# Kernel optimization log

Measured on AMD Instinct MI355X. Metric: run time of the kernel, lower is better.

Reference implementation:

```python
import jax, jax.numpy as jnp
import numpy as np

N_AGENTS, BATCH, SDIM, ADIM = 8, 16384, 64, 16
HID, HEADS = 128, 4
ATT_D = HID // HEADS  # 32
EPS = 1e-5


def _bn(x):
    # BatchNorm1d(affine=False), training-mode stats over batch axis (axis=1), biased var
    m = x.mean(axis=1, keepdims=True)
    v = ((x - m) ** 2).mean(axis=1, keepdims=True)
    return (x - m) * jax.lax.rsqrt(v + EPS)


def setup_inputs() -> dict:
    key = jax.random.key(0)
    ks = jax.random.split(key, 16)
    sc = lambda *sh: 1.0 / np.sqrt(sh[-2] if len(sh) > 1 else sh[-1])
    inp = {
        "s": jax.random.normal(ks[0], (N_AGENTS, BATCH, SDIM), jnp.float32),
        "a": jax.random.uniform(ks[1], (N_AGENTS, BATCH, ADIM), jnp.float32),
        # per-agent sa encoder (Attention_Actor): Linear(sdim+adim, hid)
        "W_sa": jax.random.normal(ks[2], (N_AGENTS, SDIM + ADIM, HID), jnp.float32) * (1.0 / np.sqrt(SDIM + ADIM)),
        "b_sa": jnp.zeros((N_AGENTS, HID), jnp.float32),
        # per-agent state encoder: Linear(sdim, hid)
        "W_se": jax.random.normal(ks[3], (N_AGENTS, SDIM, HID), jnp.float32) * (1.0 / np.sqrt(SDIM)),
        "b_se": jnp.zeros((N_AGENTS, HID), jnp.float32),
        # per-head key/selector (no bias) and value (with bias) extractors, shared across agents
        "Wk": jax.random.normal(ks[4], (HEADS, HID, ATT_D), jnp.float32) * (1.0 / np.sqrt(HID)),
        "Wsel": jax.random.normal(ks[5], (HEADS, HID, ATT_D), jnp.float32) * (1.0 / np.sqrt(HID)),
        "Wv": jax.random.normal(ks[6], (HEADS, HID, ATT_D), jnp.float32) * (1.0 / np.sqrt(HID)),
        "bv": jnp.zeros((HEADS, ATT_D), jnp.float32),
        # per-agent critic: Linear(2*hid, hid) -> LeakyReLU -> Linear(hid, adim)
        "Wc1": jax.random.normal(ks[7], (N_AGENTS, 2 * HID, HID), jnp.float32) * (1.0 / np.sqrt(2 * HID)),
        "bc1": jnp.zeros((N_AGENTS, HID), jnp.float32),
        "Wc2": jax.random.normal(ks[8], (N_AGENTS, HID, ADIM), jnp.float32) * (1.0 / np.sqrt(HID)),
        "bc2": jnp.zeros((N_AGENTS, ADIM), jnp.float32),
    }
    return inp


def reference(s, a, W_sa, b_sa, W_se, b_se, Wk, Wsel, Wv, bv, Wc1, bc1, Wc2, bc2):
    lrelu = jax.nn.leaky_relu  # slope 0.01 like nn.LeakyReLU default
    # sa encodings: BN -> Linear -> LeakyReLU, per agent  [N,B,H]
    sa = _bn(jnp.concatenate([s, a], axis=-1))
    e = lrelu(jnp.einsum('nbi,nih->nbh', sa, W_sa) + b_sa[:, None, :])
    # state encodings  [N,B,H]
    se = lrelu(jnp.einsum('nbi,nih->nbh', _bn(s), W_se) + b_se[:, None, :])
    # per-head projections  [P,N,B,D]
    keys = jnp.einsum('nbh,phd->pnbd', e, Wk)
    vals = lrelu(jnp.einsum('nbh,phd->pnbd', e, Wv) + bv[:, None, None, :])
    sel = jnp.einsum('nbh,phd->pnbd', se, Wsel)
    # attention of agent i over agents j != i  [P,N,N,B]
    logits = jnp.einsum('pibd,pjbd->pijb', sel, keys) / np.sqrt(ATT_D).astype(np.float32)
    self_mask = jnp.eye(N_AGENTS, dtype=bool)[None, :, :, None]
    w = jax.nn.softmax(jnp.where(self_mask, -1e9, logits), axis=2)
    other = jnp.einsum('pijb,pjbd->pibd', w, vals)  # [P,N,B,D]
    other_flat = jnp.transpose(other, (1, 2, 0, 3)).reshape(N_AGENTS, BATCH, HEADS * ATT_D)
    # critic: concat(s_enc, head values) -> MLP -> gather Q at argmax action
    critic_in = jnp.concatenate([se, other_flat], axis=-1)  # [N,B,2H]
    h = lrelu(jnp.einsum('nbi,nih->nbh', critic_in, Wc1) + bc1[:, None, :])
    all_q = jnp.einsum('nbh,nho->nbo', h, Wc2) + bc2[:, None, :]  # [N,B,adim]
    int_acs = jnp.argmax(a, axis=-1)[..., None]  # [N,B,1]
    q = jnp.take_along_axis(all_q, int_acs, axis=-1)  # [N,B,1]
    return q
```

## Files before the change

kernel.cpp:

```cpp
#include <hip/hip_runtime.h>


typedef unsigned short u16;
typedef unsigned int u32;

#define NA 8
#define BATCH 16384
#define SD 64
#define AD 16
#define IND 80
#define HID 128
#define HEADS 4
#define ATT 32
#define EPS 1e-5f
#define KP 136
#define KP3 104
#define KPS 72
#define SP 34
#define VTS2 136
#define WBS 24

using short8 = __attribute__((ext_vector_type(8))) short;
using float4f = __attribute__((ext_vector_type(4))) float;
using uint4v = __attribute__((ext_vector_type(4))) u32;
#define MFMA16(a, b, c) __builtin_amdgcn_mfma_f32_16x16x32_bf16((a), (b), (c), 0, 0, 0)

__device__ __forceinline__ float bf2f(u16 u) { union { u32 i; float f; } v; v.i = ((u32)u) << 16; return v.f; }
__device__ __forceinline__ float lo2f(u32 w) { union { u32 i; float f; } v; v.i = w << 16; return v.f; }
__device__ __forceinline__ float hi2f(u32 w) { union { u32 i; float f; } v; v.i = w & 0xffff0000u; return v.f; }
__device__ __forceinline__ u16 f2bf(float f) {
  union { float f; u32 i; } v; v.f = f;
  u32 x = v.i;
  x += 0x7fffu + ((x >> 16) & 1u);
  return (u16)(x >> 16);
}
__device__ __forceinline__ float lrelu(float x) { return x > 0.f ? x : 0.01f * x; }
__device__ __forceinline__ float ldin(const void* p, size_t i, bool bf) {
  return bf ? bf2f(((const u16*)p)[i]) : ((const float*)p)[i];
}
__device__ __forceinline__ u16 ldbf(const void* p, size_t i, bool bf) {
  return bf ? ((const u16*)p)[i] : f2bf(((const float*)p)[i]);
}
__device__ __forceinline__ short8 lds_s8(const u16* p) {
  union { short8 v; u32 u[4]; } t;
  const u32* q = (const u32*)p;
  t.u[0] = q[0]; t.u[1] = q[1]; t.u[2] = q[2]; t.u[3] = q[3];
  return t.v;
}
__device__ __forceinline__ void barlg() {
  asm volatile("s_waitcnt lgkmcnt(0)" ::: "memory");
  __builtin_amdgcn_s_barrier();
}

__global__ __launch_bounds__(256) void k_prep2(
    const void* __restrict__ s, const void* __restrict__ a,
    const void* __restrict__ Wsa, const void* __restrict__ Wse,
    const void* __restrict__ Wsl, const void* __restrict__ Wk, const void* __restrict__ Wv,
    const void* __restrict__ Wc1,
    int* __restrict__ flag, float* __restrict__ part,
    u16* __restrict__ Wsa_t, u16* __restrict__ Wse_t, u16* __restrict__ Wp_t, u16* __restrict__ Wc1t) {
  __shared__ u16 T[80 * 130];
  __shared__ float S0[256], Q0[256], S1[256], Q1[256];
  __shared__ int cnt[2];
  int tid = threadIdx.x;
  if (tid < 2) cnt[tid] = 0;
  __syncthreads();
  {
    u32 wv = ((const u32*)s)[tid];
    u32 lo = wv & 0xffffu, e = (lo >> 7) & 0xffu;
    if (lo == 0u || lo == 0x8000u) atomicAdd(&cnt[1], 1);
    else if (e < 0x70u || e > 0x8fu) atomicAdd(&cnt[0], 1);
  }
  __syncthreads();
  bool bf = !(cnt[0] >= 64 || cnt[1] >= 192);
  if (blockIdx.x == 0 && tid == 0) *flag = bf ? 1 : 0;
  int blkr = blockIdx.x;
  if (blkr < 2048) {
    int n = blkr >> 8, c = blkr & 255, b0 = c << 6;
    float* p = part + (size_t)(n * 256 + c) * 160;
    {
      int f2 = tid & 31, rg = tid >> 5;
      float s0 = 0.f, s1 = 0.f, q0 = 0.f, q1 = 0.f;
      #pragma unroll
      for (int i = 0; i < 8; i++) {
        int b = b0 + rg + 8 * i;
        float x0, x1;
        if (bf) { u32 wv = ((const u32*)s)[((size_t)n * BATCH + b) * 32 + f2]; x0 = lo2f(wv); x1 = hi2f(wv); }
        else { const float* sf = (const float*)s + ((size_t)n * BATCH + b) * 64 + 2 * f2; x0 = sf[0]; x1 = sf[1]; }
        s0 += x0; q0 += x0 * x0; s1 += x1; q1 += x1 * x1;
      }
      S0[tid] = s0; Q0[tid] = q0; S1[tid] = s1; Q1[tid] = q1;
    }
    __syncthreads();
    if (tid < 64) {
      int f2 = tid >> 1, odd = tid & 1;
      float S = 0.f, Q = 0.f;
      #pragma unroll
      for (int rg = 0; rg < 8; rg++) {
        int ix = rg * 32 + f2;
        S += odd ? S1[ix] : S0[ix];
        Q += odd ? Q1[ix] : Q0[ix];
      }
      p[tid * 2] = S; p[tid * 2 + 1] = Q;
    }
    __syncthreads();
    {
      int f2 = tid & 7, rg = tid >> 3;
      float s0 = 0.f, s1 = 0.f, q0 = 0.f, q1 = 0.f;
      #pragma unroll
      for (int i = 0; i < 2; i++) {
        int b = b0 + rg + 32 * i;
        float x0, x1;
        if (bf) { u32 wv = ((const u32*)a)[((size_t)n * BATCH + b) * 8 + f2]; x0 = lo2f(wv); x1 = hi2f(wv); }
        else { const float* af = (const float*)a + ((size_t)n * BATCH + b) * 16 + 2 * f2; x0 = af[0]; x1 = af[1]; }
        s0 += x0; q0 += x0 * x0; s1 += x1; q1 += x1 * x1;
      }
      S0[tid] = s0; Q0[tid] = q0; S1[tid] = s1; Q1[tid] = q1;
    }
    __syncthreads();
    if (tid < 16) {
      int f2 = tid >> 1, odd = tid & 1;
      float S = 0.f, Q = 0.f;
      #pragma unroll
      for (int rg = 0; rg < 32; rg++) {
        int ix = rg * 8 + f2;
        S += odd ? S1[ix] : S0[ix];
        Q += odd ? Q1[ix] : Q0[ix];
      }
      p[(SD + tid) * 2] = S; p[(SD + tid) * 2 + 1] = Q;
    }
    return;
  }
  int blk = blkr - 2048;
  if (blk < 32) {
    int n = blk >> 2, k0 = (blk & 3) * 64;
    for (int i = tid; i < 64 * 128; i += 256) {
      int kr = i >> 7, cc = i & 127;
      T[kr * 130 + cc] = ldbf(Wc1, ((size_t)n * 256 + k0 + kr) * 128 + cc, bf);
    }
    __syncthreads();
    for (int i = tid; i < 128 * 64; i += 256) {
      int col = i >> 6, kk = i & 63;
      Wc1t[((size_t)n * 128 + col) * 256 + k0 + kk] = T[kk * 130 + col];
    }
  } else if (blk < 40) {
    int n = blk - 32;
    for (int i = tid; i < 80 * 128; i += 256) {
      int kr = i >> 7, cc = i & 127;
      T[kr * 130 + cc] = ldbf(Wsa, ((size_t)n * IND + kr) * 128 + cc, bf);
    }
    __syncthreads();
    for (int i = tid; i < 128 * KP3; i += 256) {
      int col = i / KP3, k = i - col * KP3;
      Wsa_t[((size_t)n * 128 + col) * KP3 + k] = (k < IND) ? T[k * 130 + col] : (u16)0;
    }
  } else if (blk < 48) {
    int n = blk - 40;
    for (int i = tid; i < 64 * 128; i += 256) {
      int kr = i >> 7, cc = i & 127;
      T[kr * 130 + cc] = ldbf(Wse, ((size_t)n * SD + kr) * 128 + cc, bf);
    }
    __syncthreads();
    for (int i = tid; i < 128 * KPS; i += 256) {
      int col = i / KPS, k = i - col * KPS;
      Wse_t[((size_t)n * 128 + col) * KPS + k] = (k < SD) ? T[k * 130 + col] : (u16)0;
    }
  } else {
    int pm = blk - 48, p = pm / 3, mat = pm - 3 * p;
    const void* W = (mat == 0) ? Wsl : (mat == 1) ? Wk : Wv;
    for (int i = tid; i < 128 * 32; i += 256) {
      int kr = i >> 5, d = i & 31;
      T[kr * 34 + d] = ldbf(W, ((size_t)p * HID + kr) * ATT + d, bf);
    }
    __syncthreads();
    for (int i = tid; i < 32 * KP; i += 256) {
      int d = i / KP, k = i - d * KP;
      Wp_t[((size_t)mat * HID + p * ATT + d) * KP + k] = (k < HID) ? T[k * 34 + d] : (u16)0;
    }
  }
}

__global__ __launch_bounds__(256) void k_fin(const float* __restrict__ part, float* __restrict__ mst_g) {
  int n = blockIdx.x;
  int t = threadIdx.x;
  if (t < 160) {
    const float* p = part + (size_t)n * 256 * 160 + t;
    float acc = 0.f;
    #pragma unroll 8
    for (int c = 0; c < 256; c++) acc += p[(size_t)c * 160];
    float other = __shfl_xor(acc, 1);
    if ((t & 1) == 0) {
      float mean = acc * (1.f / BATCH);
      float var = other * (1.f / BATCH) - mean * mean;
      mst_g[(size_t)n * 160 + t] = mean;
      mst_g[(size_t)n * 160 + t + 1] = rsqrtf(var + EPS);
    }
  }
}

__global__ __launch_bounds__(512, 4) void k_fused(
    const void* __restrict__ s, const void* __restrict__ a,
    const u16* __restrict__ Wsa_t, const void* __restrict__ bsa,
    const u16* __restrict__ Wse_t, const void* __restrict__ bse,
    const u16* __restrict__ Wp_t, const void* __restrict__ bv_g,
    const float* __restrict__ mst_g, const int* __restrict__ flag,
    u16* __restrict__ SEo, u16* __restrict__ OT2) {
  __shared__ __align__(16) u16 A[128 * KP];
  __shared__ __align__(16) u16 scr[128 * SP];
  __shared__ __align__(16) u16 valt[ATT * VTS2];
  __shared__ u16 wb[128 * WBS];
  __shared__ float mst[NA * 160];
  bool bf = (*flag != 0);
  int tid = threadIdx.x;
  int B0 = blockIdx.x * 16;
  int w = tid >> 6, lane = tid & 63, q = lane >> 4, rl = lane & 15;
  for (int i = tid; i < NA * 160; i += 512) mst[i] = mst_g[i];
  barlg();
  for (int i = tid; i < 128 * 32; i += 512) {
    int row = i >> 5, kp = i & 31;
    int ag = row >> 4, bi = row & 15;
    float x0, x1;
    if (bf) { u32 wv = ((const u32*)s)[((size_t)ag * BATCH + B0 + bi) * 32 + kp]; x0 = lo2f(wv); x1 = hi2f(wv); }
    else { const float* sf = (const float*)s + ((size_t)ag * BATCH + B0 + bi) * 64 + 2 * kp; x0 = sf[0]; x1 = sf[1]; }
    int k = 2 * kp;
    const float* m = &mst[ag * 160];
    u32 o = (u32)f2bf((x0 - m[k * 2]) * m[k * 2 + 1]) |
            ((u32)f2bf((x1 - m[k * 2 + 2]) * m[k * 2 + 3]) << 16);
    *(u32*)&A[row * KP + k] = o;
  }
  for (int i = tid; i < 128 * 8; i += 512) {
    int row = i >> 3, kp = i & 7;
    int ag = row >> 4, bi = row & 15;
    float x0, x1;
    if (bf) { u32 wv = ((const u32*)a)[((size_t)ag * BATCH + B0 + bi) * 8 + kp]; x0 = lo2f(wv); x1 = hi2f(wv); }
    else { const float* af = (const float*)a + ((size_t)ag * BATCH + B0 + bi) * 16 + 2 * kp; x0 = af[0]; x1 = af[1]; }
    int k = SD + 2 * kp;
    const float* m = &mst[ag * 160];
    u32 o = (u32)f2bf((x0 - m[k * 2]) * m[k * 2 + 1]) |
            ((u32)f2bf((x1 - m[k * 2 + 2]) * m[k * 2 + 3]) << 16);
    *(u32*)&A[row * KP + k] = o;
  }
  for (int i = tid; i < 128 * 8; i += 512) {
    int row = i >> 3, c2 = i & 7;
    *(u32*)&A[row * KP + IND + 2 * c2] = 0u;
  }
  barlg();
  const int n = w;
  const u16* WS = Wse_t + (size_t)n * HID * KPS;
  const u16* WA = Wsa_t + (size_t)n * HID * KP3;
  float4f accS[8] = {};
  #pragma unroll
  for (int kc = 0; kc < 2; kc++) {
    short8 a0 = *(const short8*)&A[(w * 16 + rl) * KP + kc * 32 + q * 8];
    #pragma unroll
    for (int nt = 0; nt < 8; nt++) {
      short8 bb = *(const short8*)(WS + (size_t)(nt * 16 + rl) * KPS + kc * 32 + q * 8);
      accS[nt] = MFMA16(a0, bb, accS[nt]);
    }
  }
  float4f accE[8] = {};
  #pragma unroll
  for (int kc = 0; kc < 3; kc++) {
    short8 a0 = *(const short8*)&A[(w * 16 + rl) * KP + kc * 32 + q * 8];
    #pragma unroll
    for (int nt = 0; nt < 8; nt++) {
      short8 bb = *(const short8*)(WA + (size_t)(nt * 16 + rl) * KP3 + kc * 32 + q * 8);
      accE[nt] = MFMA16(a0, bb, accE[nt]);
    }
  }
  barlg();
  #pragma unroll
  for (int nt = 0; nt < 8; nt++) {
    int col = nt * 16 + rl;
    float bias = ldin(bse, n * HID + col, bf);
    #pragma unroll
    for (int r = 0; r < 4; r++) {
      int bi = q * 4 + r;
      u16 v = f2bf(lrelu(accS[nt][r] + bias));
      A[(w * 16 + bi) * KP + col] = v;
      SEo[((size_t)n * BATCH + B0 + bi) * HID + col] = v;
    }
  }
  const u16* WSL = Wp_t;
  const u16* WKm = Wp_t + (size_t)HID * KP;
  const u16* WVm = Wp_t + (size_t)2 * HID * KP;
  short8 saf[HEADS];
  #pragma unroll
  for (int p = 0; p < HEADS; p++) {
    float4f ac[2] = {};
    #pragma unroll
    for (int kc = 0; kc < 4; kc++) {
      short8 af = *(const short8*)&A[(w * 16 + rl) * KP + kc * 32 + q * 8];
      #pragma unroll
      for (int nt = 0; nt < 2; nt++) {
        short8 bl = *(const short8*)(WSL + (size_t)(p * ATT + nt * 16 + rl) * KP + kc * 32 + q * 8);
        ac[nt] = MFMA16(af, bl, ac[nt]);
      }
    }
    #pragma unroll
    for (int nt = 0; nt < 2; nt++)
      #pragma unroll
      for (int r = 0; r < 4; r++) {
        int bi = q * 4 + r, d = nt * 16 + rl;
        scr[(bi * 8 + w) * SP + d] = f2bf(ac[nt][r]);
      }
    barlg();
    saf[p] = lds_s8(&scr[(w * 16 + rl) * SP + q * 8]);
    barlg();
  }
  #pragma unroll
  for (int nt = 0; nt < 8; nt++) {
    int col = nt * 16 + rl;
    float bias = ldin(bsa, n * HID + col, bf);
    #pragma unroll
    for (int r = 0; r < 4; r++)
      A[(w * 16 + q * 4 + r) * KP + col] = f2bf(lrelu(accE[nt][r] + bias));
  }
  const float scale = 0.17677669529663687f;
  #pragma unroll
  for (int p = 0; p < HEADS; p++) {
    float4f ak[2] = {}, av[2] = {};
    #pragma unroll
    for (int kc = 0; kc < 4; kc++) {
      short8 af = *(const short8*)&A[(w * 16 + rl) * KP + kc * 32 + q * 8];
      #pragma unroll
      for (int nt = 0; nt < 2; nt++) {
        short8 bk = *(const short8*)(WKm + (size_t)(p * ATT + nt * 16 + rl) * KP + kc * 32 + q * 8);
        ak[nt] = MFMA16(af, bk, ak[nt]);
        short8 bv8 = *(const short8*)(WVm + (size_t)(p * ATT + nt * 16 + rl) * KP + kc * 32 + q * 8);
        av[nt] = MFMA16(af, bv8, av[nt]);
      }
    }
    #pragma unroll
    for (int nt = 0; nt < 2; nt++) {
      int d = nt * 16 + rl;
      float bvv = ldin(bv_g, p * ATT + d, bf);
      #pragma unroll
      for (int r = 0; r < 4; r++) {
        int bi = q * 4 + r, iRow = bi * 8 + w;
        scr[iRow * SP + d] = f2bf(ak[nt][r]);
        valt[d * VTS2 + iRow] = f2bf(lrelu(av[nt][r] + bvv));
      }
    }
    barlg();
    short8 sa = saf[p];
    short8 kb = lds_s8(&scr[(w * 16 + rl) * SP + q * 8]);
    float4f zc = {};
    float4f c = MFMA16(sa, kb, zc);
    int nn = rl;
    #pragma unroll
    for (int r = 0; r < 4; r++) {
      int row = q * 4 + r;
      float x = c[r] * scale;
      if (row == nn) x = -1e9f;
      float mx = x;
      mx = fmaxf(mx, __shfl_xor(mx, 1));
      mx = fmaxf(mx, __shfl_xor(mx, 2));
      mx = fmaxf(mx, __shfl_xor(mx, 4));
      float e = __expf(x - mx);
      float ssum = e;
      ssum += __shfl_xor(ssum, 1);
      ssum += __shfl_xor(ssum, 2);
      ssum += __shfl_xor(ssum, 4);
      float wv = e / ssum;
      if ((row >> 3) != (nn >> 3)) wv = 0.f;
      wb[(w * 16 + row) * WBS + nn] = f2bf(wv);
    }
    short8 aw;
    if (q < 2) aw = *(const short8*)&wb[(w * 16 + rl) * WBS + q * 8];
    else { short8 z = {}; aw = z; }
    float4f o[2] = {};
    #pragma unroll
    for (int nt = 0; nt < 2; nt++) {
      short8 bv8 = lds_s8(&valt[(nt * 16 + rl) * VTS2 + w * 16 + (q & 1) * 8]);
      o[nt] = MFMA16(aw, bv8, o[nt]);
    }
    #pragma unroll
    for (int nt = 0; nt < 2; nt++)
      #pragma unroll
      for (int r = 0; r < 4; r++) {
        int row = q * 4 + r;
        int rp = w * 16 + (row >> 3) * 8 + (row & 7);
        OT2[((size_t)blockIdx.x * 128 + rp) * HID + p * ATT + nt * 16 + rl] = f2bf(o[nt][r]);
      }
    barlg();
  }
}

__global__ __launch_bounds__(256) void k_critic2(
    const u16* __restrict__ SEi, const u16* __restrict__ OT, const void* __restrict__ a_g,
    const u16* __restrict__ Wc1t, const void* __restrict__ bc1_g,
    const void* __restrict__ Wc2_g, const void* __restrict__ bc2_g,
    const int* __restrict__ flag, void* __restrict__ qo) {
  __shared__ __align__(16) u16 Xt[128 * KP];
  __shared__ float wc2f[HID * AD];
  __shared__ float bc1f[HID];
  __shared__ int amax[128];
  bool bf = (*flag != 0);
  int tid = threadIdx.x;
  int n = blockIdx.y;
  int b0 = blockIdx.x * 128;
  int w = tid >> 6, lane = tid & 63, q = lane >> 4, rl = lane & 15;
  if (tid < HID) bc1f[tid] = ldin(bc1_g, n * HID + tid, bf);
  {
    int b = tid >> 1, half = tid & 1;
    float best; int bi;
    if (bf) {
      const uint4v* pa = (const uint4v*)((const u32*)a_g + ((size_t)n * BATCH + b0 + b) * 8 + half * 4);
      uint4v x = *pa;
      float v[8] = {lo2f(x[0]), hi2f(x[0]), lo2f(x[1]), hi2f(x[1]),
                    lo2f(x[2]), hi2f(x[2]), lo2f(x[3]), hi2f(x[3])};
      best = v[0]; bi = 0;
      #pragma unroll
      for (int j = 1; j < 8; j++) if (v[j] > best) { best = v[j]; bi = j; }
    } else {
      const float* pa = (const float*)a_g + ((size_t)n * BATCH + b0 + b) * 16 + half * 8;
      float4f v0 = *(const float4f*)pa, v1 = *(const float4f*)(pa + 4);
      float v[8] = {v0[0], v0[1], v0[2], v0[3], v1[0], v1[1], v1[2], v1[3]};
      best = v[0]; bi = 0;
      #pragma unroll
      for (int j = 1; j < 8; j++) if (v[j] > best) { best = v[j]; bi = j; }
    }
    float ob = __shfl_xor(best, 1);
    int obi = __shfl_xor(bi, 1);
    if (half == 0) amax[b] = (ob > best) ? (obi + 8) : bi;
  }
  for (int idx = tid; idx < HID * AD; idx += 256)
    wc2f[idx] = ldin(Wc2_g, (size_t)n * HID * AD + idx, bf);
  const u16* WT = Wc1t + (size_t)n * HID * 256;

  float4f acc[8][2] = {};
  for (int ph = 0; ph < 2; ph++) {
    for (int idx = tid; idx < 128 * 64; idx += 256) {
      int row = idx >> 6, c = idx & 63;
      u32 wv;
      if (ph == 0) wv = ((const u32*)SEi)[((size_t)n * BATCH + b0 + row) * 64 + c];
      else         wv = ((const u32*)OT)[((size_t)(b0 + row) * NA + n) * 64 + c];
      ((u32*)&Xt[row * KP])[c] = wv;
    }
    barlg();
    #pragma unroll
    for (int kc = 0; kc < 4; kc++) {
      int ko = ph * HID + kc * 32;
      short8 bb0 = *(const short8*)(WT + (size_t)(w * 32 + rl) * 256 + ko + q * 8);
      short8 bb1 = *(const short8*)(WT + (size_t)(w * 32 + 16 + rl) * 256 + ko + q * 8);
      #pragma unroll
      for (int mt = 0; mt < 8; mt++) {
        short8 af = *(const short8*)&Xt[(mt * 16 + rl) * KP + kc * 32 + q * 8];
        acc[mt][0] = MFMA16(af, bb0, acc[mt][0]);
        acc[mt][1] = MFMA16(af, bb1, acc[mt][1]);
      }
    }
    barlg();
  }
  u16* ht = Xt;
  #pragma unroll
  for (int mt = 0; mt < 8; mt++)
    #pragma unroll
    for (int nt = 0; nt < 2; nt++)
      #pragma unroll
      for (int r = 0; r < 4; r++) {
        int row = mt * 16 + q * 4 + r, col = w * 32 + nt * 16 + rl;
        ht[row * KP + col] = f2bf(lrelu(acc[mt][nt][r] + bc1f[col]));
      }
  barlg();
  {
    int b = tid >> 1, half = tid & 1;
    int col = amax[b];
    float acq = 0.f;
    const u16* hr = &ht[b * KP + half * 64];
    const float* wz = &wc2f[(half * 64) * AD + col];
    #pragma unroll
    for (int kk = 0; kk < 8; kk++) {
      short8 hv = lds_s8(hr + kk * 8);
      #pragma unroll
      for (int j = 0; j < 8; j++)
        acq = fmaf(bf2f((u16)hv[j]), wz[(kk * 8 + j) * AD], acq);
    }
    acq += __shfl_xor(acq, 1);
    if (half == 0) {
      float v = acq + ldin(bc2_g, n * AD + col, bf);
      size_t oidx = (size_t)n * BATCH + b0 + b;
      if (bf) ((u16*)qo)[oidx] = f2bf(v);
      else    ((float*)qo)[oidx] = v;
    }
  }
}

extern "C" void kernel_launch(void* const* d_in, const int* in_sizes, int n_in,
                              void* d_out, int out_size, void* d_ws, size_t ws_size,
                              hipStream_t stream) {
  const void* s   = d_in[0];
  const void* a   = d_in[1];
  const void* Wsa = d_in[2];
  const void* bsa = d_in[3];
  const void* Wse = d_in[4];
  const void* bse = d_in[5];
  const void* Wk  = d_in[6];
  const void* Wsl = d_in[7];
  const void* Wv  = d_in[8];
  const void* bv  = d_in[9];
  const void* Wc1 = d_in[10];
  const void* bc1 = d_in[11];
  const void* Wc2 = d_in[12];
  const void* bc2 = d_in[13];

  char* ws = (char*)d_ws;
  int*   flag  = (int*)ws;
  float* part  = (float*)(ws + 1024);
  float* mst_g = (float*)(ws + 1311744);
  u16*   Wsa_t = (u16*)(ws + 1316864);
  u16*   Wse_t = (u16*)(ws + 1529856);
  u16*   Wp_t  = (u16*)(ws + 1677312);
  u16*   Wc1t  = (u16*)(ws + 1781760);
  u16*   SEb   = (u16*)(ws + 2306048);
  u16*   OT2   = (u16*)(ws + 2306048 + 1ull * 33554432ull);

  k_prep2<<<2108, 256, 0, stream>>>(s, a, Wsa, Wse, Wsl, Wk, Wv, Wc1,
                                    flag, part, Wsa_t, Wse_t, Wp_t, Wc1t);
  k_fin<<<NA, 256, 0, stream>>>(part, mst_g);
  k_fused<<<BATCH / 16, 512, 0, stream>>>(s, a, Wsa_t, bsa, Wse_t, bse, Wp_t, bv,
                                          mst_g, flag, SEb, OT2);
  k_critic2<<<dim3(BATCH / 128, NA), 256, 0, stream>>>(SEb, OT2, a, Wc1t, bc1, Wc2, bc2, flag, d_out);
}
```

Baseline: 256.3 us.

## Batch all head projections in fused kernel to cut per-head barriers

Restructures the fused attention kernel so the selector, key and value projections for all four heads are computed up front in register accumulators. The results are staged once into two full-size LDS buffers, replacing the small per-head scratch and value-transpose buffers. This removes the two or three block barriers per head and lets each A-fragment load feed all head MFMAs. In exchange, register pressure rises sharply (24 float4 accumulators plus the earlier ones), which could cause spills or lower occupancy under the 512-thread, 4-block launch bound. LDS footprint also grows.

```diff
diff --git a/kernel.cpp b/kernel.cpp
--- a/kernel.cpp
+++ b/kernel.cpp
@@ -16,8 +16,6 @@
 #define KP 136
 #define KP3 104
 #define KPS 72
-#define SP 34
-#define VTS2 136
 #define WBS 24
 
 using short8 = __attribute__((ext_vector_type(8))) short;
@@ -198,7 +196,7 @@
   }
 }
 
-__global__ __launch_bounds__(512, 4) void k_fused(
+__global__ __launch_bounds__(512, 4) void k_fused2(
     const void* __restrict__ s, const void* __restrict__ a,
     const u16* __restrict__ Wsa_t, const void* __restrict__ bsa,
     const u16* __restrict__ Wse_t, const void* __restrict__ bse,
@@ -206,8 +204,7 @@
     const float* __restrict__ mst_g, const int* __restrict__ flag,
     u16* __restrict__ SEo, u16* __restrict__ OT2) {
   __shared__ __align__(16) u16 A[128 * KP];
-  __shared__ __align__(16) u16 scr[128 * SP];
-  __shared__ __align__(16) u16 valt[ATT * VTS2];
+  __shared__ __align__(16) u16 Bt[128 * KP];
   __shared__ u16 wb[128 * WBS];
   __shared__ float mst[NA * 160];
   bool bf = (*flag != 0);
@@ -272,79 +269,81 @@
   #pragma unroll
   for (int nt = 0; nt < 8; nt++) {
     int col = nt * 16 + rl;
-    float bias = ldin(bse, n * HID + col, bf);
+    float biasS = ldin(bse, n * HID + col, bf);
+    float biasE = ldin(bsa, n * HID + col, bf);
     #pragma unroll
     for (int r = 0; r < 4; r++) {
       int bi = q * 4 + r;
-      u16 v = f2bf(lrelu(accS[nt][r] + bias));
-      A[(w * 16 + bi) * KP + col] = v;
+      u16 v = f2bf(lrelu(accS[nt][r] + biasS));
+      Bt[(w * 16 + bi) * KP + col] = v;
       SEo[((size_t)n * BATCH + B0 + bi) * HID + col] = v;
+      A[(w * 16 + bi) * KP + col] = f2bf(lrelu(accE[nt][r] + biasE));
     }
   }
   const u16* WSL = Wp_t;
   const u16* WKm = Wp_t + (size_t)HID * KP;
   const u16* WVm = Wp_t + (size_t)2 * HID * KP;
-  short8 saf[HEADS];
-  #pragma unroll
-  for (int p = 0; p < HEADS; p++) {
-    float4f ac[2] = {};
-    #pragma unroll
-    for (int kc = 0; kc < 4; kc++) {
-      short8 af = *(const short8*)&A[(w * 16 + rl) * KP + kc * 32 + q * 8];
+  float4f aSL[4][2] = {};
+  #pragma unroll
+  for (int kc = 0; kc < 4; kc++) {
+    short8 af = *(const short8*)&Bt[(w * 16 + rl) * KP + kc * 32 + q * 8];
+    #pragma unroll
+    for (int p = 0; p < HEADS; p++)
       #pragma unroll
       for (int nt = 0; nt < 2; nt++) {
         short8 bl = *(const short8*)(WSL + (size_t)(p * ATT + nt * 16 + rl) * KP + kc * 32 + q * 8);
-        ac[nt] = MFMA16(af, bl, ac[nt]);
-      }
-    }
-    #pragma unroll
-    for (int nt = 0; nt < 2; nt++)
-      #pragma unroll
-      for (int r = 0; r < 4; r++) {
-        int bi = q * 4 + r, d = nt * 16 + rl;
-        scr[(bi * 8 + w) * SP + d] = f2bf(ac[nt][r]);
-      }
-    barlg();
-    saf[p] = lds_s8(&scr[(w * 16 + rl) * SP + q * 8]);
-    barlg();
-  }
-  #pragma unroll
-  for (int nt = 0; nt < 8; nt++) {
-    int col = nt * 16 + rl;
-    float bias = ldin(bsa, n * HID + col, bf);
-    #pragma unroll
-    for (int r = 0; r < 4; r++)
-      A[(w * 16 + q * 4 + r) * KP + col] = f2bf(lrelu(accE[nt][r] + bias));
-  }
-  const float scale = 0.17677669529663687f;
-  #pragma unroll
-  for (int p = 0; p < HEADS; p++) {
-    float4f ak[2] = {}, av[2] = {};
-    #pragma unroll
-    for (int kc = 0; kc < 4; kc++) {
-      short8 af = *(const short8*)&A[(w * 16 + rl) * KP + kc * 32 + q * 8];
+        aSL[p][nt] = MFMA16(af, bl, aSL[p][nt]);
+      }
+  }
+  float4f aK[4][2] = {}, aV[4][2] = {};
+  #pragma unroll
+  for (int kc = 0; kc < 4; kc++) {
+    short8 af = *(const short8*)&A[(w * 16 + rl) * KP + kc * 32 + q * 8];
+    #pragma unroll
+    for (int p = 0; p < HEADS; p++)
       #pragma unroll
       for (int nt = 0; nt < 2; nt++) {
         short8 bk = *(const short8*)(WKm + (size_t)(p * ATT + nt * 16 + rl) * KP + kc * 32 + q * 8);
-        ak[nt] = MFMA16(af, bk, ak[nt]);
+        aK[p][nt] = MFMA16(af, bk, aK[p][nt]);
         short8 bv8 = *(const short8*)(WVm + (size_t)(p * ATT + nt * 16 + rl) * KP + kc * 32 + q * 8);
-        av[nt] = MFMA16(af, bv8, av[nt]);
-      }
-    }
+        aV[p][nt] = MFMA16(af, bv8, aV[p][nt]);
+      }
+  }
+  barlg();
+  #pragma unroll
+  for (int p = 0; p < HEADS; p++)
+    #pragma unroll
+    for (int nt = 0; nt < 2; nt++)
+      #pragma unroll
+      for (int r = 0; r < 4; r++) {
+        int iRow = (q * 4 + r) * 8 + w, col = p * ATT + nt * 16 + rl;
+        Bt[iRow * KP + col] = f2bf(aSL[p][nt][r]);
+        A[iRow * KP + col] = f2bf(aK[p][nt][r]);
+      }
+  barlg();
+  short8 saf[HEADS];
+  #pragma unroll
+  for (int p = 0; p < HEADS; p++)
+    saf[p] = lds_s8(&Bt[(w * 16 + rl) * KP + p * ATT + q * 8]);
+  barlg();
+  #pragma unroll
+  for (int p = 0; p < HEADS; p++)
     #pragma unroll
     for (int nt = 0; nt < 2; nt++) {
       int d = nt * 16 + rl;
       float bvv = ldin(bv_g, p * ATT + d, bf);
       #pragma unroll
       for (int r = 0; r < 4; r++) {
-        int bi = q * 4 + r, iRow = bi * 8 + w;
-        scr[iRow * SP + d] = f2bf(ak[nt][r]);
-        valt[d * VTS2 + iRow] = f2bf(lrelu(av[nt][r] + bvv));
-      }
-    }
-    barlg();
+        int iRow = (q * 4 + r) * 8 + w;
+        Bt[(p * ATT + d) * KP + iRow] = f2bf(lrelu(aV[p][nt][r] + bvv));
+      }
+    }
+  barlg();
+  const float scale = 0.17677669529663687f;
+  #pragma unroll
+  for (int p = 0; p < HEADS; p++) {
     short8 sa = saf[p];
-    short8 kb = lds_s8(&scr[(w * 16 + rl) * SP + q * 8]);
+    short8 kb = lds_s8(&A[(w * 16 + rl) * KP + p * ATT + q * 8]);
     float4f zc = {};
     float4f c = MFMA16(sa, kb, zc);
     int nn = rl;
@@ -372,7 +371,7 @@
     float4f o[2] = {};
     #pragma unroll
     for (int nt = 0; nt < 2; nt++) {
-      short8 bv8 = lds_s8(&valt[(nt * 16 + rl) * VTS2 + w * 16 + (q & 1) * 8]);
+      short8 bv8 = lds_s8(&Bt[(p * ATT + nt * 16 + rl) * KP + w * 16 + (q & 1) * 8]);
       o[nt] = MFMA16(aw, bv8, o[nt]);
     }
     #pragma unroll
@@ -383,7 +382,6 @@
         int rp = w * 16 + (row >> 3) * 8 + (row & 7);
         OT2[((size_t)blockIdx.x * 128 + rp) * HID + p * ATT + nt * 16 + rl] = f2bf(o[nt][r]);
       }
-    barlg();
   }
 }
 
@@ -519,7 +517,7 @@
   k_prep2<<<2108, 256, 0, stream>>>(s, a, Wsa, Wse, Wsl, Wk, Wv, Wc1,
                                     flag, part, Wsa_t, Wse_t, Wp_t, Wc1t);
   k_fin<<<NA, 256, 0, stream>>>(part, mst_g);
-  k_fused<<<BATCH / 16, 512, 0, stream>>>(s, a, Wsa_t, bsa, Wse_t, bse, Wp_t, bv,
-                                          mst_g, flag, SEb, OT2);
+  k_fused2<<<BATCH / 16, 512, 0, stream>>>(s, a, Wsa_t, bsa, Wse_t, bse, Wp_t, bv,
+                                           mst_g, flag, SEb, OT2);
   k_critic2<<<dim3(BATCH / 128, NA), 256, 0, stream>>>(SEb, OT2, a, Wc1t, bc1, Wc2, bc2, flag, d_out);
 }
```

Result: slower. 320.5 us (+25.1%).
